# Optimization experiments

Hardware: AMD Instinct MI355X
Metric: run time of the kernel (lower is better)

The kernel has to match this reference:

```python
import jax, jax.numpy as jnp
import numpy as np
from jax import lax

EPS = 1e-5
NUM_GROUPS = 32
OFFSET_SCALE = 1.0
K = 3            # deformable conv kernel size
KK = K * K
DWK = 7          # depthwise kernel size for offset predictor


def group_norm(x, gamma, beta, num_groups=NUM_GROUPS):
    B, C, H, W = x.shape
    xg = x.reshape(B, num_groups, C // num_groups, H, W)
    m = xg.mean(axis=(2, 3, 4), keepdims=True)
    v = xg.var(axis=(2, 3, 4), keepdims=True)
    xn = ((xg - m) * lax.rsqrt(v + EPS)).reshape(B, C, H, W)
    return xn * gamma[None, :, None, None] + beta[None, :, None, None]


def bilinear_gather(x, py, px):
    # x: [B,C,H,W]; py, px: [B,KK,H,W] absolute sample coords -> [B,C,KK,H,W]
    B, C, H, W = x.shape
    y0 = jnp.floor(py)
    x0 = jnp.floor(px)
    wy1 = py - y0
    wx1 = px - x0
    wy0 = 1.0 - wy1
    wx0 = 1.0 - wx1
    xf = x.reshape(B, C, H * W)

    def gather(yi, xi):
        valid = (yi >= 0) & (yi <= H - 1) & (xi >= 0) & (xi <= W - 1)
        yc = jnp.clip(yi, 0, H - 1).astype(jnp.int32)
        xc = jnp.clip(xi, 0, W - 1).astype(jnp.int32)
        idx = (yc * W + xc).reshape(B, -1)                      # [B, KK*H*W]
        g = jax.vmap(lambda a, i: a[:, i])(xf, idx)             # [B, C, KK*H*W]
        g = g.reshape(B, C, KK, H, W)
        return g * valid.astype(x.dtype)[:, None]

    out = (gather(y0, x0) * (wy0 * wx0)[:, None]
           + gather(y0, x0 + 1.0) * (wy0 * wx1)[:, None]
           + gather(y0 + 1.0, x0) * (wy1 * wx0)[:, None]
           + gather(y0 + 1.0, x0 + 1.0) * (wy1 * wx1)[:, None])
    return out


def deform_conv(x, dw, pw, pwb, w, b):
    # x: [B,C,H,W]; dw: [C,1,DWK,DWK] depthwise; pw: [2*KK,C,1,1]; w: [O,C,K,K]
    B, C, H, W = x.shape
    dn = ('NCHW', 'OIHW', 'NCHW')
    f = lax.conv_general_dilated(x, dw, (1, 1), 'SAME',
                                 feature_group_count=C, dimension_numbers=dn)
    off = lax.conv_general_dilated(f, pw, (1, 1), 'SAME', dimension_numbers=dn)
    off = (off + pwb[None, :, None, None]) * OFFSET_SCALE       # [B,2*KK,H,W]
    off = off.reshape(B, KK, 2, H, W)
    ks = jnp.arange(K, dtype=x.dtype) - (K - 1) / 2             # [-1,0,1]
    ky = jnp.repeat(ks, K)                                      # [KK]
    kx = jnp.tile(ks, K)
    yy, xx = jnp.meshgrid(jnp.arange(H, dtype=x.dtype),
                          jnp.arange(W, dtype=x.dtype), indexing='ij')
    py = yy[None, None] + ky[None, :, None, None] + off[:, :, 0]  # [B,KK,H,W]
    px = xx[None, None] + kx[None, :, None, None] + off[:, :, 1]
    sampled = bilinear_gather(x, py, px)                        # [B,C,KK,H,W]
    O = w.shape[0]
    out = jnp.einsum('bckhw,ock->bohw', sampled, w.reshape(O, C, KK))
    return out + b[None, :, None, None]


def setup_inputs() -> dict:
    key = jax.random.key(0)
    ks = jax.random.split(key, 10)
    B, C, H, W = 4, 256, 64, 64
    O = C
    x = jax.random.normal(ks[0], (B, C, H, W), dtype=jnp.float32)

    def conv_w(k, shape, fan_in):
        return jax.random.normal(k, shape, dtype=jnp.float32) / np.sqrt(fan_in)

    inp = {
        'x': x,
        'gn1_g': jnp.ones((C,), jnp.float32), 'gn1_b': jnp.zeros((C,), jnp.float32),
        'dw1': conv_w(ks[1], (C, 1, DWK, DWK), DWK * DWK),
        'pw1': jax.random.normal(ks[2], (2 * KK, C, 1, 1), jnp.float32) * 0.01,
        'pwb1': jnp.zeros((2 * KK,), jnp.float32),
        'w1': conv_w(ks[3], (O, C, K, K), C * KK),
        'b1': jnp.zeros((O,), jnp.float32),
        'gn2_g': jnp.ones((O,), jnp.float32), 'gn2_b': jnp.zeros((O,), jnp.float32),
        'dw2': conv_w(ks[4], (O, 1, DWK, DWK), DWK * DWK),
        'pw2': jax.random.normal(ks[5], (2 * KK, O, 1, 1), jnp.float32) * 0.01,
        'pwb2': jnp.zeros((2 * KK,), jnp.float32),
        'w2': conv_w(ks[6], (O, O, K, K), O * KK),
        'b2': jnp.zeros((O,), jnp.float32),
    }
    return inp


def reference(x, gn1_g, gn1_b, dw1, pw1, pwb1, w1, b1,
              gn2_g, gn2_b, dw2, pw2, pwb2, w2, b2):
    h = jax.nn.relu(group_norm(x, gn1_g, gn1_b))
    h = deform_conv(h, dw1, pw1, pwb1, w1, b1)
    h = jax.nn.relu(group_norm(h, gn2_g, gn2_b))
    # Dropout / DropPath are identity in eval mode
    h = deform_conv(h, dw2, pw2, pwb2, w2, b2)
    return h + x  # shortcut is Identity (in_channels == out_channels)
```

## Files before the change

### kernel.cpp

```cpp
#include <hip/hip_runtime.h>

#define B_    4
#define C_    256
#define H_    64
#define W_    64
#define HW_   4096
#define NG_   32
#define CPG_  8
#define KK_   9
#define NOFF_ 18

typedef __attribute__((ext_vector_type(8))) short short8;
typedef __attribute__((ext_vector_type(4))) short short4v;
typedef __attribute__((ext_vector_type(4))) float floatx4;

static __device__ __forceinline__ short f2bf(float f) {
    union { float f; unsigned u; } v; v.f = f;
    unsigned r = v.u + 0x7fff + ((v.u >> 16) & 1);
    return (short)(r >> 16);
}
static __device__ __forceinline__ float bf2f(short s) {
    union { unsigned u; float f; } v;
    v.u = ((unsigned)(unsigned short)s) << 16;
    return v.f;
}

__global__ __launch_bounds__(1024) void gn_relu_kernel(
    const float* __restrict__ in, const float* __restrict__ gamma,
    const float* __restrict__ beta, short* __restrict__ outb)
{
    int b = blockIdx.x >> 5;
    int g = blockIdx.x & 31;
    const int N = CPG_ * HW_;
    size_t base = ((size_t)(b * C_ + g * CPG_)) * HW_;
    const float4* in4 = (const float4*)(in + base);
    int t = threadIdx.x;

    float s = 0.f, ss = 0.f;
    for (int i = t; i < N / 4; i += 1024) {
        float4 v = in4[i];
        s  += v.x + v.y + v.z + v.w;
        ss += v.x * v.x + v.y * v.y + v.z * v.z + v.w * v.w;
    }
    #pragma unroll
    for (int off = 32; off > 0; off >>= 1) {
        s  += __shfl_down(s, off, 64);
        ss += __shfl_down(ss, off, 64);
    }
    __shared__ float red[32];
    __shared__ float sh_rs, sh_m;
    int wid = t >> 6;
    if ((t & 63) == 0) { red[wid] = s; red[16 + wid] = ss; }
    __syncthreads();
    if (t == 0) {
        float S = 0.f, SS = 0.f;
        #pragma unroll
        for (int i = 0; i < 16; ++i) { S += red[i]; SS += red[16 + i]; }
        float m = S / (float)N;
        float var = SS / (float)N - m * m;
        sh_rs = rsqrtf(var + 1e-5f);
        sh_m = m;
    }
    __syncthreads();
    float rs = sh_rs, m = sh_m;
    short4v* out4 = (short4v*)(outb + base);
    for (int i = t; i < N / 4; i += 1024) {
        int ch = g * CPG_ + (i >> 10);
        float ga = gamma[ch] * rs;
        float be = beta[ch] - m * ga;
        float4 v = in4[i];
        short4v o;
        o.x = f2bf(fmaxf(fmaf(v.x, ga, be), 0.f));
        o.y = f2bf(fmaxf(fmaf(v.y, ga, be), 0.f));
        o.z = f2bf(fmaxf(fmaf(v.z, ga, be), 0.f));
        o.w = f2bf(fmaxf(fmaf(v.w, ga, be), 0.f));
        out4[i] = o;
    }
}

__global__ __launch_bounds__(256) void dw7t_kernel(
    const short* __restrict__ in, const float* __restrict__ dwk,
    short* __restrict__ fdw, short* __restrict__ hbt)
{
    int plane = blockIdx.x;
    int b = plane >> 8;
    int c = plane & (C_ - 1);
    const short* src = in + (size_t)plane * HW_;
    __shared__ float tile[70 * 72];
    __shared__ float wk[49];
    int t = threadIdx.x;
    if (t < 49) wk[t] = dwk[c * 49 + t];
    for (int i = t; i < 70 * 72; i += 256) tile[i] = 0.f;
    __syncthreads();
    const short4v* src4 = (const short4v*)src;
    short* hb = hbt + ((size_t)b * HW_) * C_ + c;
    for (int i = t; i < HW_ / 4; i += 256) {
        short4v v = src4[i];
        int y = i >> 4, x = (i & 15) * 4;
        float* tp = &tile[(y + 3) * 72 + (x + 3)];
        tp[0] = bf2f(v.x); tp[1] = bf2f(v.y);
        tp[2] = bf2f(v.z); tp[3] = bf2f(v.w);
        int px = i * 4;
        hb[(size_t)px * C_]       = v.x;
        hb[(size_t)(px + 1) * C_] = v.y;
        hb[(size_t)(px + 2) * C_] = v.z;
        hb[(size_t)(px + 3) * C_] = v.w;
    }
    __syncthreads();
    short* fb = fdw + ((size_t)b * HW_) * C_ + c;
    #pragma unroll
    for (int it = 0; it < 4; ++it) {
        int idx = it * 256 + t;
        int y = idx >> 4;
        int x0 = (idx & 15) * 4;
        float a0 = 0.f, a1 = 0.f, a2 = 0.f, a3 = 0.f;
        #pragma unroll
        for (int dy = 0; dy < 7; ++dy) {
            const float* tr = &tile[(y + dy) * 72 + x0];
            float4 ra = *(const float4*)tr;
            float4 rb = *(const float4*)(tr + 4);
            float4 rc = *(const float4*)(tr + 8);
            float r[12] = {ra.x, ra.y, ra.z, ra.w,
                           rb.x, rb.y, rb.z, rb.w,
                           rc.x, rc.y, rc.z, rc.w};
            const float* wr = &wk[dy * 7];
            #pragma unroll
            for (int dx = 0; dx < 7; ++dx) {
                float wv = wr[dx];
                a0 = fmaf(r[dx], wv, a0);
                a1 = fmaf(r[dx + 1], wv, a1);
                a2 = fmaf(r[dx + 2], wv, a2);
                a3 = fmaf(r[dx + 3], wv, a3);
            }
        }
        size_t ob = (size_t)(y * 64 + x0) * C_;
        fb[ob]          = f2bf(a0);
        fb[ob + C_]     = f2bf(a1);
        fb[ob + 2 * C_] = f2bf(a2);
        fb[ob + 3 * C_] = f2bf(a3);
    }
}

__global__ __launch_bounds__(256) void wpack_all_kernel(
    const float* __restrict__ w1, const float* __restrict__ w2,
    const float* __restrict__ pw1, const float* __restrict__ pw2,
    short* __restrict__ wp1, short* __restrict__ wp2,
    short* __restrict__ ppk1, short* __restrict__ ppk2)
{
    int blk = blockIdx.x;
    if (blk < 4608) {
        const float* w = (blk < 2304) ? w1 : w2;
        short* wp = (blk < 2304) ? wp1 : wp2;
        int idx = (blk & 2047) * 256 + ((blk & 2048) ? 524288 : 0) + threadIdx.x;
        idx = (blk % 2304) * 256 + threadIdx.x;
        int j    = idx & 7;
        int lane = (idx >> 3) & 63;
        int ot   = (idx >> 9) & 15;
        int slab = idx >> 13;
        int k = slab >> 3, cc = slab & 7;
        int o = ot * 16 + (lane & 15);
        int c = cc * 32 + (lane >> 4) * 8 + j;
        wp[idx] = f2bf(w[(size_t)(o * C_ + c) * KK_ + k]);
    } else {
        int q = blk - 4608;
        const float* pw = (q < 32) ? pw1 : pw2;
        short* ppk = (q < 32) ? ppk1 : ppk2;
        int idx = (q & 31) * 256 + threadIdx.x;
        int j = idx & 7, lane = (idx >> 3) & 63;
        int ot = (idx >> 9) & 1, sl = idx >> 10;
        int o = ot * 16 + (lane & 15);
        int k = sl * 32 + (lane >> 4) * 8 + j;
        ppk[idx] = (o < NOFF_) ? f2bf(pw[o * C_ + k]) : (short)0;
    }
}

__global__ __launch_bounds__(1024) void deform_fused_kernel(
    const short* __restrict__ ht,   const short* __restrict__ fdw,
    const short* __restrict__ ppk,  const float* __restrict__ pwb,
    const short* __restrict__ wp,   const float* __restrict__ bias,
    const float* __restrict__ resid, float* __restrict__ out)
{
    int b = blockIdx.x >> 6;
    int row = blockIdx.x & 63;
    __shared__ int   i00[576], i01[576], i10[576], i11[576];
    __shared__ float c00[576], c01[576], c10[576], c11[576];
    __shared__ float off_lds[NOFF_ * 64];
    __shared__ __align__(16) short sbuf[2][16384];
    int t = threadIdx.x;
    int wv = t >> 6, lane = t & 63;
    int pq = lane >> 4, pr = lane & 15;

    if (wv < 8) {
        int ot = wv & 1, ptw = wv >> 1;
        int px = ptw * 16 + pr;
        const short8* fb8 = (const short8*)(fdw +
            ((size_t)b * HW_ + row * 64 + px) * C_);
        const short8* ap = (const short8*)ppk;
        floatx4 pacc = (floatx4){0.f, 0.f, 0.f, 0.f};
        #pragma unroll
        for (int sl = 0; sl < 8; ++sl) {
            short8 af = ap[(sl * 2 + ot) * 64 + lane];
            short8 bf = fb8[sl * 4 + pq];
            pacc = __builtin_amdgcn_mfma_f32_16x16x32_bf16(af, bf, pacc, 0, 0, 0);
        }
        #pragma unroll
        for (int r = 0; r < 4; ++r) {
            int o = ot * 16 + pq * 4 + r;
            if (o < NOFF_) off_lds[o * 64 + px] = pacc[r] + pwb[o];
        }
    }
    __syncthreads();

    if (t < 576) {
        int e = t;
        int k = e >> 6, p = e & 63;
        float offy = off_lds[(2 * k) * 64 + p];
        float offx = off_lds[(2 * k + 1) * 64 + p];
        float py = (float)row + (float)(k / 3 - 1) + offy;
        float px = (float)p   + (float)(k % 3 - 1) + offx;
        float y0f = floorf(py), x0f = floorf(px);
        float wy1 = py - y0f, wx1 = px - x0f;
        float wy0 = 1.f - wy1, wx0 = 1.f - wx1;
        float y1f = y0f + 1.f, x1f = x0f + 1.f;
        bool vy0 = (y0f >= 0.f) && (y0f <= 63.f);
        bool vy1 = (y1f >= 0.f) && (y1f <= 63.f);
        bool vx0 = (x0f >= 0.f) && (x0f <= 63.f);
        bool vx1 = (x1f >= 0.f) && (x1f <= 63.f);
        int iy0 = (int)fminf(fmaxf(y0f, 0.f), 63.f);
        int iy1 = (int)fminf(fmaxf(y1f, 0.f), 63.f);
        int ix0 = (int)fminf(fmaxf(x0f, 0.f), 63.f);
        int ix1 = (int)fminf(fmaxf(x1f, 0.f), 63.f);
        i00[e] = iy0 * 64 + ix0; i01[e] = iy0 * 64 + ix1;
        i10[e] = iy1 * 64 + ix0; i11[e] = iy1 * 64 + ix1;
        c00[e] = (vy0 && vx0) ? wy0 * wx0 : 0.f;
        c01[e] = (vy0 && vx1) ? wy0 * wx1 : 0.f;
        c10[e] = (vy1 && vx0) ? wy1 * wx0 : 0.f;
        c11[e] = (vy1 && vx1) ? wy1 * wx1 : 0.f;
    }
    __syncthreads();

    int scb = t & 3, spx = (t >> 2) & 63, ssl0 = t >> 8;
    int u2 = spx * 4 + (scb ^ ((spx + (spx >> 2)) & 3));
    const short* hb = ht + ((size_t)b * HW_) * C_;
    const short* hb0 = hb + ssl0 * 32 + scb * 8;
    const short* hb1 = hb + (ssl0 + 4) * 32 + scb * 8;

    short8 ra[4], rb[4];
    auto prefetch = [&](int g) {
        int e = g * 64 + spx;
        int a00 = i00[e], a01 = i01[e], a10 = i10[e], a11 = i11[e];
        ra[0] = *(const short8*)(hb0 + (size_t)a00 * C_);
        ra[1] = *(const short8*)(hb0 + (size_t)a01 * C_);
        ra[2] = *(const short8*)(hb0 + (size_t)a10 * C_);
        ra[3] = *(const short8*)(hb0 + (size_t)a11 * C_);
        rb[0] = *(const short8*)(hb1 + (size_t)a00 * C_);
        rb[1] = *(const short8*)(hb1 + (size_t)a01 * C_);
        rb[2] = *(const short8*)(hb1 + (size_t)a10 * C_);
        rb[3] = *(const short8*)(hb1 + (size_t)a11 * C_);
    };
    auto stage_write = [&](int g, int bi) {
        int e = g * 64 + spx;
        float w00 = c00[e], w01 = c01[e], w10 = c10[e], w11 = c11[e];
        short8 va, vb;
        #pragma unroll
        for (int j = 0; j < 8; ++j) {
            va[j] = f2bf(w00 * bf2f(ra[0][j]) + w01 * bf2f(ra[1][j])
                       + w10 * bf2f(ra[2][j]) + w11 * bf2f(ra[3][j]));
            vb[j] = f2bf(w00 * bf2f(rb[0][j]) + w01 * bf2f(rb[1][j])
                       + w10 * bf2f(rb[2][j]) + w11 * bf2f(rb[3][j]));
        }
        *(short8*)&sbuf[bi][ssl0 * 2048 + u2 * 8] = va;
        *(short8*)&sbuf[bi][(ssl0 + 4) * 2048 + u2 * 8] = vb;
    };

    floatx4 acc[4];
    #pragma unroll
    for (int pt = 0; pt < 4; ++pt) acc[pt] = (floatx4){0.f, 0.f, 0.f, 0.f};
    int ub[4];
    #pragma unroll
    for (int pt = 0; pt < 4; ++pt) {
        int px2 = pt * 16 + pr;
        ub[pt] = px2 * 4 + (pq ^ ((px2 + (px2 >> 2)) & 3));
    }

    prefetch(0);
    stage_write(0, 0);
    prefetch(1);
    __syncthreads();

    const short8* wp8 = (const short8*)wp;
    for (int g = 0; g < 9; ++g) {
        const short* sb = sbuf[g & 1];
        #pragma unroll
        for (int half = 0; half < 2; ++half) {
            short8 af[4];
            #pragma unroll
            for (int q = 0; q < 4; ++q)
                af[q] = wp8[(size_t)((g * 8 + half * 4 + q) * 16 + wv) * 64 + lane];
            #pragma unroll
            for (int q = 0; q < 4; ++q) {
                int sl = half * 4 + q;
                #pragma unroll
                for (int pt = 0; pt < 4; ++pt) {
                    short8 bfv = *(const short8*)&sb[sl * 2048 + ub[pt] * 8];
                    acc[pt] = __builtin_amdgcn_mfma_f32_16x16x32_bf16(
                        af[q], bfv, acc[pt], 0, 0, 0);
                }
            }
        }
        if (g + 1 < 9) {
            stage_write(g + 1, (g + 1) & 1);
            if (g + 2 < 9) prefetch(g + 2);
        }
        __syncthreads();
    }

    #pragma unroll
    for (int r = 0; r < 4; ++r) {
        int o = wv * 16 + pq * 4 + r;
        float bo = bias[o];
        size_t obase = ((size_t)(b * C_ + o)) * HW_ + row * 64 + pr;
        #pragma unroll
        for (int pt = 0; pt < 4; ++pt) {
            float v = acc[pt][r] + bo;
            if (resid) v += resid[obase + pt * 16];
            out[obase + pt * 16] = v;
        }
    }
}

extern "C" void kernel_launch(void* const* d_in, const int* in_sizes, int n_in,
                              void* d_out, int out_size, void* d_ws, size_t ws_size,
                              hipStream_t stream)
{
    const float* x     = (const float*)d_in[0];
    const float* gn1_g = (const float*)d_in[1];
    const float* gn1_b = (const float*)d_in[2];
    const float* dw1   = (const float*)d_in[3];
    const float* pw1   = (const float*)d_in[4];
    const float* pwb1  = (const float*)d_in[5];
    const float* w1    = (const float*)d_in[6];
    const float* b1    = (const float*)d_in[7];
    const float* gn2_g = (const float*)d_in[8];
    const float* gn2_b = (const float*)d_in[9];
    const float* dw2   = (const float*)d_in[10];
    const float* pw2   = (const float*)d_in[11];
    const float* pwb2  = (const float*)d_in[12];
    const float* w2    = (const float*)d_in[13];
    const float* b2    = (const float*)d_in[14];
    float* out = (float*)d_out;

    float* ws   = (float*)d_ws;
    float* y1   = ws;
    short* hbf  = (short*)(ws + 4194304);
    short* hbt  = (short*)(ws + 6291456);
    short* fdw  = (short*)(ws + 8388608);
    short* wp1  = (short*)(ws + 10485760);
    short* wp2  = (short*)(ws + 10780672);
    short* ppk1 = (short*)(ws + 11075584);
    short* ppk2 = (short*)(ws + 11079680);

    wpack_all_kernel<<<4672, 256, 0, stream>>>(w1, w2, pw1, pw2,
                                               wp1, wp2, ppk1, ppk2);

    gn_relu_kernel<<<B_ * NG_, 1024, 0, stream>>>(x, gn1_g, gn1_b, hbf);
    dw7t_kernel<<<B_ * C_, 256, 0, stream>>>(hbf, dw1, fdw, hbt);
    deform_fused_kernel<<<B_ * H_, 1024, 0, stream>>>(
        hbt, fdw, ppk1, pwb1, wp1, b1, nullptr, y1);

    gn_relu_kernel<<<B_ * NG_, 1024, 0, stream>>>(y1, gn2_g, gn2_b, hbf);
    dw7t_kernel<<<B_ * C_, 256, 0, stream>>>(hbf, dw2, fdw, hbt);
    deform_fused_kernel<<<B_ * H_, 1024, 0, stream>>>(
        hbt, fdw, ppk2, pwb2, wp2, b2, x, out);
}
```

Baseline: 291.7 us.

## Restructure pipeline: fuse GN stats into prep and conv epilogue, split deform blocks

Folds the GroupNorm-1 statistics into the weight-pack prep kernel. GroupNorm-2 statistics are accumulated with atomics in the first deform-conv epilogue, which now writes the intermediate in bf16 instead of fp32. A new gnt kernel does normalize+ReLU and produces both the planar and the transposed bf16 tensors through an LDS-swizzled tile, replacing the scattered 2-byte transposed writes in the depthwise kernel. The depthwise conv output stays planar, the deform kernel transposes it through LDS, and the grid is split into half-row blocks (512 instead of 256). Risks include atomic nondeterminism, extra precision loss from the bf16 intermediate, and less work per block in the MFMA loop.

```diff
diff --git a/kernel.cpp b/kernel.cpp
--- a/kernel.cpp
+++ b/kernel.cpp
@@ -25,67 +25,157 @@
     return v.f;
 }
 
-__global__ __launch_bounds__(1024) void gn_relu_kernel(
-    const float* __restrict__ in, const float* __restrict__ gamma,
-    const float* __restrict__ beta, short* __restrict__ outb)
+__global__ __launch_bounds__(256) void prep_kernel(
+    const float* __restrict__ w1, const float* __restrict__ w2,
+    const float* __restrict__ pw1, const float* __restrict__ pw2,
+    const float* __restrict__ x,
+    short* __restrict__ wp1, short* __restrict__ wp2,
+    short* __restrict__ ppk1, short* __restrict__ ppk2,
+    float2* __restrict__ stats1, float* __restrict__ gsum,
+    float* __restrict__ gss)
 {
-    int b = blockIdx.x >> 5;
-    int g = blockIdx.x & 31;
-    const int N = CPG_ * HW_;
-    size_t base = ((size_t)(b * C_ + g * CPG_)) * HW_;
-    const float4* in4 = (const float4*)(in + base);
+    int blk = blockIdx.x;
     int t = threadIdx.x;
-
-    float s = 0.f, ss = 0.f;
-    for (int i = t; i < N / 4; i += 1024) {
-        float4 v = in4[i];
-        s  += v.x + v.y + v.z + v.w;
-        ss += v.x * v.x + v.y * v.y + v.z * v.z + v.w * v.w;
-    }
+    if (blk < 4608) {
+        const float* w = (blk < 2304) ? w1 : w2;
+        short* wp = (blk < 2304) ? wp1 : wp2;
+        int idx = (blk % 2304) * 256 + t;
+        int j    = idx & 7;
+        int lane = (idx >> 3) & 63;
+        int ot   = (idx >> 9) & 15;
+        int slab = idx >> 13;
+        int k = slab >> 3, cc = slab & 7;
+        int o = ot * 16 + (lane & 15);
+        int c = cc * 32 + (lane >> 4) * 8 + j;
+        wp[idx] = f2bf(w[(size_t)(o * C_ + c) * KK_ + k]);
+    } else if (blk < 4672) {
+        int q = blk - 4608;
+        const float* pw = (q < 32) ? pw1 : pw2;
+        short* ppk = (q < 32) ? ppk1 : ppk2;
+        int idx = (q & 31) * 256 + t;
+        int j = idx & 7, lane = (idx >> 3) & 63;
+        int ot = (idx >> 9) & 1, sl = idx >> 10;
+        int o = ot * 16 + (lane & 15);
+        int k = sl * 32 + (lane >> 4) * 8 + j;
+        ppk[idx] = (o < NOFF_) ? f2bf(pw[o * C_ + k]) : (short)0;
+    } else if (blk < 4800) {
+        int q = blk - 4672;
+        size_t base = (size_t)q * CPG_ * HW_;
+        const float4* in4 = (const float4*)(x + base);
+        float s = 0.f, ss = 0.f;
+        for (int i = t; i < 8192; i += 256) {
+            float4 v = in4[i];
+            s  += v.x + v.y + v.z + v.w;
+            ss += v.x * v.x + v.y * v.y + v.z * v.z + v.w * v.w;
+        }
+        #pragma unroll
+        for (int d = 32; d > 0; d >>= 1) {
+            s  += __shfl_down(s, d, 64);
+            ss += __shfl_down(ss, d, 64);
+        }
+        __shared__ float red[8];
+        int wid = t >> 6;
+        if ((t & 63) == 0) { red[wid] = s; red[4 + wid] = ss; }
+        __syncthreads();
+        if (t == 0) {
+            float S  = red[0] + red[1] + red[2] + red[3];
+            float SS = red[4] + red[5] + red[6] + red[7];
+            float m = S / 32768.f;
+            float var = SS / 32768.f - m * m;
+            stats1[q] = make_float2(m, rsqrtf(var + 1e-5f));
+        }
+    } else {
+        if (t < 128) { gsum[t] = 0.f; gss[t] = 0.f; }
+    }
+}
+
+__global__ __launch_bounds__(256) void gnt_kernel(
+    const float* __restrict__ xin, const short* __restrict__ yin,
+    const float2* __restrict__ stats1, const float* __restrict__ gsum,
+    const float* __restrict__ gss, const float* __restrict__ gamma,
+    const float* __restrict__ beta, short* __restrict__ hbf,
+    short* __restrict__ hbt, int layer)
+{
+    int q = blockIdx.x;
+    int b = q >> 6;
+    int px0 = (q & 63) * 64;
+    __shared__ unsigned ltile[64 * 132];
+    __shared__ float2 sst[32];
+    int t = threadIdx.x;
+    if (t < 32) {
+        float m, rs;
+        if (layer == 1) { float2 v = stats1[b * 32 + t]; m = v.x; rs = v.y; }
+        else {
+            float s = gsum[b * 32 + t], ss = gss[b * 32 + t];
+            m = s / 32768.f;
+            float var = ss / 32768.f - m * m;
+            rs = rsqrtf(var + 1e-5f);
+        }
+        sst[t] = make_float2(m, rs);
+    }
+    __syncthreads();
+    int pq4 = t & 15, cphi = t >> 4;
     #pragma unroll
-    for (int off = 32; off > 0; off >>= 1) {
-        s  += __shfl_down(s, off, 64);
-        ss += __shfl_down(ss, off, 64);
-    }
-    __shared__ float red[32];
-    __shared__ float sh_rs, sh_m;
-    int wid = t >> 6;
-    if ((t & 63) == 0) { red[wid] = s; red[16 + wid] = ss; }
-    __syncthreads();
-    if (t == 0) {
-        float S = 0.f, SS = 0.f;
-        #pragma unroll
-        for (int i = 0; i < 16; ++i) { S += red[i]; SS += red[16 + i]; }
-        float m = S / (float)N;
-        float var = SS / (float)N - m * m;
-        sh_rs = rsqrtf(var + 1e-5f);
-        sh_m = m;
-    }
-    __syncthreads();
-    float rs = sh_rs, m = sh_m;
-    short4v* out4 = (short4v*)(outb + base);
-    for (int i = t; i < N / 4; i += 1024) {
-        int ch = g * CPG_ + (i >> 10);
-        float ga = gamma[ch] * rs;
-        float be = beta[ch] - m * ga;
-        float4 v = in4[i];
-        short4v o;
-        o.x = f2bf(fmaxf(fmaf(v.x, ga, be), 0.f));
-        o.y = f2bf(fmaxf(fmaf(v.y, ga, be), 0.f));
-        o.z = f2bf(fmaxf(fmaf(v.z, ga, be), 0.f));
-        o.w = f2bf(fmaxf(fmaf(v.w, ga, be), 0.f));
-        out4[i] = o;
-    }
-}
-
-__global__ __launch_bounds__(256) void dw7t_kernel(
+    for (int i = 0; i < 8; ++i) {
+        int cp = i * 16 + cphi;
+        int c0 = 2 * cp, c1 = c0 + 1;
+        float2 st = sst[c0 >> 3];
+        float ga0 = gamma[c0] * st.y, be0 = beta[c0] - st.x * ga0;
+        float ga1 = gamma[c1] * st.y, be1 = beta[c1] - st.x * ga1;
+        short4v lo, hi;
+        if (layer == 1) {
+            const float* r0 = xin + (size_t)(b * C_ + c0) * HW_ + px0 + pq4 * 4;
+            float4 v0 = *(const float4*)r0;
+            float4 v1 = *(const float4*)(r0 + HW_);
+            lo.x = f2bf(fmaxf(fmaf(v0.x, ga0, be0), 0.f));
+            lo.y = f2bf(fmaxf(fmaf(v0.y, ga0, be0), 0.f));
+            lo.z = f2bf(fmaxf(fmaf(v0.z, ga0, be0), 0.f));
+            lo.w = f2bf(fmaxf(fmaf(v0.w, ga0, be0), 0.f));
+            hi.x = f2bf(fmaxf(fmaf(v1.x, ga1, be1), 0.f));
+            hi.y = f2bf(fmaxf(fmaf(v1.y, ga1, be1), 0.f));
+            hi.z = f2bf(fmaxf(fmaf(v1.z, ga1, be1), 0.f));
+            hi.w = f2bf(fmaxf(fmaf(v1.w, ga1, be1), 0.f));
+        } else {
+            const short* r0 = yin + (size_t)(b * C_ + c0) * HW_ + px0 + pq4 * 4;
+            short4v v0 = *(const short4v*)r0;
+            short4v v1 = *(const short4v*)(r0 + HW_);
+            lo.x = f2bf(fmaxf(fmaf(bf2f(v0.x), ga0, be0), 0.f));
+            lo.y = f2bf(fmaxf(fmaf(bf2f(v0.y), ga0, be0), 0.f));
+            lo.z = f2bf(fmaxf(fmaf(bf2f(v0.z), ga0, be0), 0.f));
+            lo.w = f2bf(fmaxf(fmaf(bf2f(v0.w), ga0, be0), 0.f));
+            hi.x = f2bf(fmaxf(fmaf(bf2f(v1.x), ga1, be1), 0.f));
+            hi.y = f2bf(fmaxf(fmaf(bf2f(v1.y), ga1, be1), 0.f));
+            hi.z = f2bf(fmaxf(fmaf(bf2f(v1.z), ga1, be1), 0.f));
+            hi.w = f2bf(fmaxf(fmaf(bf2f(v1.w), ga1, be1), 0.f));
+        }
+        *(short4v*)(hbf + (size_t)(b * C_ + c0) * HW_ + px0 + pq4 * 4) = lo;
+        *(short4v*)(hbf + (size_t)(b * C_ + c1) * HW_ + px0 + pq4 * 4) = hi;
+        #pragma unroll
+        for (int j = 0; j < 4; ++j) {
+            int pl = pq4 * 4 + j;
+            unsigned wrd = (unsigned)(unsigned short)lo[j]
+                         | ((unsigned)(unsigned short)hi[j] << 16);
+            ltile[pl * 132 + (cp ^ ((pl & 7) << 2))] = wrd;
+        }
+    }
+    __syncthreads();
+    int co = t & 31, ph = t >> 5;
+    #pragma unroll
+    for (int r = 0; r < 8; ++r) {
+        int pl = r * 8 + ph;
+        uint4 v = *(const uint4*)&ltile[pl * 132 + ((co * 4) ^ ((pl & 7) << 2))];
+        *(uint4*)(hbt + ((size_t)b * HW_ + px0 + pl) * C_ + co * 8) = v;
+    }
+}
+
+__global__ __launch_bounds__(256) void dw7_kernel(
     const short* __restrict__ in, const float* __restrict__ dwk,
-    short* __restrict__ fdw, short* __restrict__ hbt)
+    short* __restrict__ out)
 {
     int plane = blockIdx.x;
-    int b = plane >> 8;
     int c = plane & (C_ - 1);
     const short* src = in + (size_t)plane * HW_;
+    short* dst = out + (size_t)plane * HW_;
     __shared__ float tile[70 * 72];
     __shared__ float wk[49];
     int t = threadIdx.x;
@@ -93,21 +183,14 @@
     for (int i = t; i < 70 * 72; i += 256) tile[i] = 0.f;
     __syncthreads();
     const short4v* src4 = (const short4v*)src;
-    short* hb = hbt + ((size_t)b * HW_) * C_ + c;
     for (int i = t; i < HW_ / 4; i += 256) {
         short4v v = src4[i];
         int y = i >> 4, x = (i & 15) * 4;
         float* tp = &tile[(y + 3) * 72 + (x + 3)];
         tp[0] = bf2f(v.x); tp[1] = bf2f(v.y);
         tp[2] = bf2f(v.z); tp[3] = bf2f(v.w);
-        int px = i * 4;
-        hb[(size_t)px * C_]       = v.x;
-        hb[(size_t)(px + 1) * C_] = v.y;
-        hb[(size_t)(px + 2) * C_] = v.z;
-        hb[(size_t)(px + 3) * C_] = v.w;
-    }
-    __syncthreads();
-    short* fb = fdw + ((size_t)b * HW_) * C_ + c;
+    }
+    __syncthreads();
     #pragma unroll
     for (int it = 0; it < 4; ++it) {
         int idx = it * 256 + t;
@@ -133,91 +216,69 @@
                 a3 = fmaf(r[dx + 3], wv, a3);
             }
         }
-        size_t ob = (size_t)(y * 64 + x0) * C_;
-        fb[ob]          = f2bf(a0);
-        fb[ob + C_]     = f2bf(a1);
-        fb[ob + 2 * C_] = f2bf(a2);
-        fb[ob + 3 * C_] = f2bf(a3);
-    }
-}
-
-__global__ __launch_bounds__(256) void wpack_all_kernel(
-    const float* __restrict__ w1, const float* __restrict__ w2,
-    const float* __restrict__ pw1, const float* __restrict__ pw2,
-    short* __restrict__ wp1, short* __restrict__ wp2,
-    short* __restrict__ ppk1, short* __restrict__ ppk2)
+        short4v o;
+        o.x = f2bf(a0); o.y = f2bf(a1); o.z = f2bf(a2); o.w = f2bf(a3);
+        *(short4v*)&dst[y * 64 + x0] = o;
+    }
+}
+
+__global__ __launch_bounds__(1024) void deform_fused_kernel(
+    const short* __restrict__ hbt,  const short* __restrict__ fdwc,
+    const short* __restrict__ ppk,  const float* __restrict__ pwb,
+    const short* __restrict__ wp,   const float* __restrict__ bias,
+    const float* __restrict__ resid, float* __restrict__ outf,
+    short* __restrict__ outb, float* __restrict__ gsum,
+    float* __restrict__ gss)
 {
     int blk = blockIdx.x;
-    if (blk < 4608) {
-        const float* w = (blk < 2304) ? w1 : w2;
-        short* wp = (blk < 2304) ? wp1 : wp2;
-        int idx = (blk & 2047) * 256 + ((blk & 2048) ? 524288 : 0) + threadIdx.x;
-        idx = (blk % 2304) * 256 + threadIdx.x;
-        int j    = idx & 7;
-        int lane = (idx >> 3) & 63;
-        int ot   = (idx >> 9) & 15;
-        int slab = idx >> 13;
-        int k = slab >> 3, cc = slab & 7;
-        int o = ot * 16 + (lane & 15);
-        int c = cc * 32 + (lane >> 4) * 8 + j;
-        wp[idx] = f2bf(w[(size_t)(o * C_ + c) * KK_ + k]);
-    } else {
-        int q = blk - 4608;
-        const float* pw = (q < 32) ? pw1 : pw2;
-        short* ppk = (q < 32) ? ppk1 : ppk2;
-        int idx = (q & 31) * 256 + threadIdx.x;
-        int j = idx & 7, lane = (idx >> 3) & 63;
-        int ot = (idx >> 9) & 1, sl = idx >> 10;
-        int o = ot * 16 + (lane & 15);
-        int k = sl * 32 + (lane >> 4) * 8 + j;
-        ppk[idx] = (o < NOFF_) ? f2bf(pw[o * C_ + k]) : (short)0;
-    }
-}
-
-__global__ __launch_bounds__(1024) void deform_fused_kernel(
-    const short* __restrict__ ht,   const short* __restrict__ fdw,
-    const short* __restrict__ ppk,  const float* __restrict__ pwb,
-    const short* __restrict__ wp,   const float* __restrict__ bias,
-    const float* __restrict__ resid, float* __restrict__ out)
-{
-    int b = blockIdx.x >> 6;
-    int row = blockIdx.x & 63;
-    __shared__ int   i00[576], i01[576], i10[576], i11[576];
-    __shared__ float c00[576], c01[576], c10[576], c11[576];
-    __shared__ float off_lds[NOFF_ * 64];
-    __shared__ __align__(16) short sbuf[2][16384];
+    int b = blk >> 7;
+    int row = (blk >> 1) & 63;
+    int ph = blk & 1;
+    __shared__ __align__(16) short sbuf[2][8192];
+    __shared__ int   pidx[288];
+    __shared__ float cf[288][4];
+    __shared__ float off_lds[NOFF_ * 32];
     int t = threadIdx.x;
     int wv = t >> 6, lane = t & 63;
     int pq = lane >> 4, pr = lane & 15;
 
-    if (wv < 8) {
+    short* ftile = &sbuf[0][0];
+    {
+        int c = t >> 2, seg = t & 3;
+        const short* src = fdwc + (size_t)(b * C_ + c) * HW_
+                         + row * 64 + ph * 32 + seg * 8;
+        *(short8*)&ftile[c * 32 + seg * 8] = *(const short8*)src;
+    }
+    __syncthreads();
+
+    if (wv < 4) {
         int ot = wv & 1, ptw = wv >> 1;
-        int px = ptw * 16 + pr;
-        const short8* fb8 = (const short8*)(fdw +
-            ((size_t)b * HW_ + row * 64 + px) * C_);
+        int pxl = ptw * 16 + pr;
         const short8* ap = (const short8*)ppk;
         floatx4 pacc = (floatx4){0.f, 0.f, 0.f, 0.f};
         #pragma unroll
         for (int sl = 0; sl < 8; ++sl) {
+            short8 bf;
+            int cbase = sl * 32 + pq * 8;
+            #pragma unroll
+            for (int j = 0; j < 8; ++j) bf[j] = ftile[(cbase + j) * 32 + pxl];
             short8 af = ap[(sl * 2 + ot) * 64 + lane];
-            short8 bf = fb8[sl * 4 + pq];
             pacc = __builtin_amdgcn_mfma_f32_16x16x32_bf16(af, bf, pacc, 0, 0, 0);
         }
         #pragma unroll
         for (int r = 0; r < 4; ++r) {
             int o = ot * 16 + pq * 4 + r;
-            if (o < NOFF_) off_lds[o * 64 + px] = pacc[r] + pwb[o];
-        }
-    }
-    __syncthreads();
-
-    if (t < 576) {
-        int e = t;
-        int k = e >> 6, p = e & 63;
-        float offy = off_lds[(2 * k) * 64 + p];
-        float offx = off_lds[(2 * k + 1) * 64 + p];
+            if (o < NOFF_) off_lds[o * 32 + pxl] = pacc[r] + pwb[o];
+        }
+    }
+    __syncthreads();
+
+    if (t < 288) {
+        int k = t >> 5, p = t & 31;
+        float offy = off_lds[(2 * k) * 32 + p];
+        float offx = off_lds[(2 * k + 1) * 32 + p];
         float py = (float)row + (float)(k / 3 - 1) + offy;
-        float px = (float)p   + (float)(k % 3 - 1) + offx;
+        float px = (float)(ph * 32 + p) + (float)(k % 3 - 1) + offx;
         float y0f = floorf(py), x0f = floorf(px);
         float wy1 = py - y0f, wx1 = px - x0f;
         float wy0 = 1.f - wy1, wx0 = 1.f - wx1;
@@ -230,55 +291,48 @@
         int iy1 = (int)fminf(fmaxf(y1f, 0.f), 63.f);
         int ix0 = (int)fminf(fmaxf(x0f, 0.f), 63.f);
         int ix1 = (int)fminf(fmaxf(x1f, 0.f), 63.f);
-        i00[e] = iy0 * 64 + ix0; i01[e] = iy0 * 64 + ix1;
-        i10[e] = iy1 * 64 + ix0; i11[e] = iy1 * 64 + ix1;
-        c00[e] = (vy0 && vx0) ? wy0 * wx0 : 0.f;
-        c01[e] = (vy0 && vx1) ? wy0 * wx1 : 0.f;
-        c10[e] = (vy1 && vx0) ? wy1 * wx0 : 0.f;
-        c11[e] = (vy1 && vx1) ? wy1 * wx1 : 0.f;
-    }
-    __syncthreads();
-
-    int scb = t & 3, spx = (t >> 2) & 63, ssl0 = t >> 8;
-    int u2 = spx * 4 + (scb ^ ((spx + (spx >> 2)) & 3));
-    const short* hb = ht + ((size_t)b * HW_) * C_;
-    const short* hb0 = hb + ssl0 * 32 + scb * 8;
-    const short* hb1 = hb + (ssl0 + 4) * 32 + scb * 8;
-
-    short8 ra[4], rb[4];
+        pidx[t] = iy0 | (ix0 << 8) | (iy1 << 16) | (ix1 << 24);
+        cf[t][0] = (vy0 && vx0) ? wy0 * wx0 : 0.f;
+        cf[t][1] = (vy0 && vx1) ? wy0 * wx1 : 0.f;
+        cf[t][2] = (vy1 && vx0) ? wy1 * wx0 : 0.f;
+        cf[t][3] = (vy1 && vx1) ? wy1 * wx1 : 0.f;
+    }
+    __syncthreads();
+
+    int sl = t >> 7;
+    int u = t & 127;
+    int pxl = u >> 2, cb = u & 3;
+    int u2 = pxl * 4 + (cb ^ ((pxl + (pxl >> 2)) & 3));
+    const short* hb0 = hbt + ((size_t)b * HW_) * C_ + sl * 32 + cb * 8;
+
+    short8 ra[4];
     auto prefetch = [&](int g) {
-        int e = g * 64 + spx;
-        int a00 = i00[e], a01 = i01[e], a10 = i10[e], a11 = i11[e];
-        ra[0] = *(const short8*)(hb0 + (size_t)a00 * C_);
-        ra[1] = *(const short8*)(hb0 + (size_t)a01 * C_);
-        ra[2] = *(const short8*)(hb0 + (size_t)a10 * C_);
-        ra[3] = *(const short8*)(hb0 + (size_t)a11 * C_);
-        rb[0] = *(const short8*)(hb1 + (size_t)a00 * C_);
-        rb[1] = *(const short8*)(hb1 + (size_t)a01 * C_);
-        rb[2] = *(const short8*)(hb1 + (size_t)a10 * C_);
-        rb[3] = *(const short8*)(hb1 + (size_t)a11 * C_);
+        int pk = pidx[g * 32 + pxl];
+        int iy0 = pk & 255, ix0 = (pk >> 8) & 255;
+        int iy1 = (pk >> 16) & 255, ix1 = (pk >> 24) & 255;
+        ra[0] = *(const short8*)(hb0 + (size_t)(iy0 * 64 + ix0) * C_);
+        ra[1] = *(const short8*)(hb0 + (size_t)(iy0 * 64 + ix1) * C_);
+        ra[2] = *(const short8*)(hb0 + (size_t)(iy1 * 64 + ix0) * C_);
+        ra[3] = *(const short8*)(hb0 + (size_t)(iy1 * 64 + ix1) * C_);
     };
     auto stage_write = [&](int g, int bi) {
-        int e = g * 64 + spx;
-        float w00 = c00[e], w01 = c01[e], w10 = c10[e], w11 = c11[e];
-        short8 va, vb;
+        int e = g * 32 + pxl;
+        float w00 = cf[e][0], w01 = cf[e][1], w10 = cf[e][2], w11 = cf[e][3];
+        short8 v8;
         #pragma unroll
         for (int j = 0; j < 8; ++j) {
-            va[j] = f2bf(w00 * bf2f(ra[0][j]) + w01 * bf2f(ra[1][j])
+            v8[j] = f2bf(w00 * bf2f(ra[0][j]) + w01 * bf2f(ra[1][j])
                        + w10 * bf2f(ra[2][j]) + w11 * bf2f(ra[3][j]));
-            vb[j] = f2bf(w00 * bf2f(rb[0][j]) + w01 * bf2f(rb[1][j])
-                       + w10 * bf2f(rb[2][j]) + w11 * bf2f(rb[3][j]));
-        }
-        *(short8*)&sbuf[bi][ssl0 * 2048 + u2 * 8] = va;
-        *(short8*)&sbuf[bi][(ssl0 + 4) * 2048 + u2 * 8] = vb;
+        }
+        *(short8*)&sbuf[bi][sl * 1024 + u2 * 8] = v8;
     };
 
-    floatx4 acc[4];
+    floatx4 acc[2];
+    acc[0] = (floatx4){0.f, 0.f, 0.f, 0.f};
+    acc[1] = (floatx4){0.f, 0.f, 0.f, 0.f};
+    int ub[2];
     #pragma unroll
-    for (int pt = 0; pt < 4; ++pt) acc[pt] = (floatx4){0.f, 0.f, 0.f, 0.f};
-    int ub[4];
-    #pragma unroll
-    for (int pt = 0; pt < 4; ++pt) {
+    for (int pt = 0; pt < 2; ++pt) {
         int px2 = pt * 16 + pr;
         ub[pt] = px2 * 4 + (pq ^ ((px2 + (px2 >> 2)) & 3));
     }
@@ -295,16 +349,16 @@
         for (int half = 0; half < 2; ++half) {
             short8 af[4];
             #pragma unroll
-            for (int q = 0; q < 4; ++q)
-                af[q] = wp8[(size_t)((g * 8 + half * 4 + q) * 16 + wv) * 64 + lane];
+            for (int q2 = 0; q2 < 4; ++q2)
+                af[q2] = wp8[(size_t)((g * 8 + half * 4 + q2) * 16 + wv) * 64 + lane];
             #pragma unroll
-            for (int q = 0; q < 4; ++q) {
-                int sl = half * 4 + q;
+            for (int q2 = 0; q2 < 4; ++q2) {
+                int s2 = half * 4 + q2;
                 #pragma unroll
-                for (int pt = 0; pt < 4; ++pt) {
-                    short8 bfv = *(const short8*)&sb[sl * 2048 + ub[pt] * 8];
+                for (int pt = 0; pt < 2; ++pt) {
+                    short8 bfv = *(const short8*)&sb[s2 * 1024 + ub[pt] * 8];
                     acc[pt] = __builtin_amdgcn_mfma_f32_16x16x32_bf16(
-                        af[q], bfv, acc[pt], 0, 0, 0);
+                        af[q2], bfv, acc[pt], 0, 0, 0);
                 }
             }
         }
@@ -315,16 +369,35 @@
         __syncthreads();
     }
 
+    float ssum = 0.f, ssq = 0.f;
     #pragma unroll
     for (int r = 0; r < 4; ++r) {
         int o = wv * 16 + pq * 4 + r;
         float bo = bias[o];
-        size_t obase = ((size_t)(b * C_ + o)) * HW_ + row * 64 + pr;
-        #pragma unroll
-        for (int pt = 0; pt < 4; ++pt) {
+        size_t obase = ((size_t)(b * C_ + o)) * HW_ + row * 64 + ph * 32 + pr;
+        #pragma unroll
+        for (int pt = 0; pt < 2; ++pt) {
             float v = acc[pt][r] + bo;
-            if (resid) v += resid[obase + pt * 16];
-            out[obase + pt * 16] = v;
+            if (outf) {
+                outf[obase + pt * 16] = v + resid[obase + pt * 16];
+            } else {
+                short sv = f2bf(v);
+                outb[obase + pt * 16] = sv;
+                float vq = bf2f(sv);
+                ssum += vq; ssq += vq * vq;
+            }
+        }
+    }
+    if (outb) {
+        #pragma unroll
+        for (int d = 1; d < 32; d <<= 1) {
+            ssum += __shfl_xor(ssum, d, 64);
+            ssq  += __shfl_xor(ssq, d, 64);
+        }
+        if ((lane & 31) == 0) {
+            int grp = wv * 2 + (pq >> 1);
+            atomicAdd(&gsum[b * 32 + grp], ssum);
+            atomicAdd(&gss[b * 32 + grp], ssq);
         }
     }
 }
@@ -351,25 +424,31 @@
     float* out = (float*)d_out;
 
     float* ws   = (float*)d_ws;
-    float* y1   = ws;
-    short* hbf  = (short*)(ws + 4194304);
-    short* hbt  = (short*)(ws + 6291456);
-    short* fdw  = (short*)(ws + 8388608);
-    short* wp1  = (short*)(ws + 10485760);
-    short* wp2  = (short*)(ws + 10780672);
-    short* ppk1 = (short*)(ws + 11075584);
-    short* ppk2 = (short*)(ws + 11079680);
-
-    wpack_all_kernel<<<4672, 256, 0, stream>>>(w1, w2, pw1, pw2,
-                                               wp1, wp2, ppk1, ppk2);
-
-    gn_relu_kernel<<<B_ * NG_, 1024, 0, stream>>>(x, gn1_g, gn1_b, hbf);
-    dw7t_kernel<<<B_ * C_, 256, 0, stream>>>(hbf, dw1, fdw, hbt);
-    deform_fused_kernel<<<B_ * H_, 1024, 0, stream>>>(
-        hbt, fdw, ppk1, pwb1, wp1, b1, nullptr, y1);
-
-    gn_relu_kernel<<<B_ * NG_, 1024, 0, stream>>>(y1, gn2_g, gn2_b, hbf);
-    dw7t_kernel<<<B_ * C_, 256, 0, stream>>>(hbf, dw2, fdw, hbt);
-    deform_fused_kernel<<<B_ * H_, 1024, 0, stream>>>(
-        hbt, fdw, ppk2, pwb2, wp2, b2, x, out);
-}
+    short* y1b    = (short*)ws;
+    short* hbf    = (short*)(ws + 2097152);
+    short* hbt    = (short*)(ws + 4194304);
+    short* fdwc   = (short*)(ws + 6291456);
+    short* wp1    = (short*)(ws + 8388608);
+    short* wp2    = (short*)(ws + 8683520);
+    short* ppk1   = (short*)(ws + 8978432);
+    short* ppk2   = (short*)(ws + 8982528);
+    float2* st1   = (float2*)(ws + 8986624);
+    float* gsum   = ws + 8986880;
+    float* gss    = ws + 8987008;
+
+    prep_kernel<<<4801, 256, 0, stream>>>(w1, w2, pw1, pw2, x,
+                                          wp1, wp2, ppk1, ppk2,
+                                          st1, gsum, gss);
+
+    gnt_kernel<<<256, 256, 0, stream>>>(x, nullptr, st1, gsum, gss,
+                                        gn1_g, gn1_b, hbf, hbt, 1);
+    dw7_kernel<<<B_ * C_, 256, 0, stream>>>(hbf, dw1, fdwc);
+    deform_fused_kernel<<<512, 1024, 0, stream>>>(
+        hbt, fdwc, ppk1, pwb1, wp1, b1, nullptr, nullptr, y1b, gsum, gss);
+
+    gnt_kernel<<<256, 256, 0, stream>>>(nullptr, y1b, st1, gsum, gss,
+                                        gn2_g, gn2_b, hbf, hbt, 2);
+    dw7_kernel<<<B_ * C_, 256, 0, stream>>>(hbf, dw2, fdwc);
+    deform_fused_kernel<<<512, 1024, 0, stream>>>(
+        hbt, fdwc, ppk2, pwb2, wp2, b2, x, out, nullptr, nullptr, nullptr);
+}
```

Measured after the change: 306.3 us. 5.0% more time.
